# Kernel optimization log

Measured on AMD Instinct MI355X. Metric: run time of the kernel, lower is better.

The kernel has to match this reference:

```python
import jax, jax.numpy as jnp
import numpy as np

N_NODES = 200000
N_EDGES = 640000
D_NODE = 128   # NO_NODE_FEATURES_TWO
D_EDGE = 32    # NO_EDGE_FEATURES_TWO
HIDDEN = 128   # HIDDEN_NODE_TWO


def setup_inputs() -> dict:
    key = jax.random.key(0)
    ks = jax.random.split(key, 8)
    x = jax.random.normal(ks[0], (N_NODES, D_NODE), dtype=jnp.float32)
    edge_index = jax.random.randint(ks[1], (2, N_EDGES), 0, N_NODES, dtype=jnp.int64)
    edge_attr = jax.random.normal(ks[2], (N_EDGES, D_EDGE), dtype=jnp.float32)
    u = jax.random.normal(ks[3], (64, D_NODE), dtype=jnp.float32)
    batch = jax.random.randint(ks[4], (N_NODES,), 0, 64, dtype=jnp.int64)
    # Xavier-uniform linear weights (stored as [in, out]); bias filled with 0.01 as in init_weights
    def xavier(k, fan_in, fan_out):
        limit = float(np.sqrt(6.0 / (fan_in + fan_out)))
        return jax.random.uniform(k, (fan_in, fan_out), jnp.float32, -limit, limit)
    W1 = xavier(ks[5], D_EDGE + D_NODE, HIDDEN)          # [160, 128]
    b1 = jnp.full((HIDDEN,), 0.01, dtype=jnp.float32)
    W2 = xavier(ks[6], HIDDEN + D_NODE, D_NODE)          # [256, 128]
    b2 = jnp.full((D_NODE,), 0.01, dtype=jnp.float32)
    return {"x": x, "edge_index": edge_index, "edge_attr": edge_attr,
            "u": u, "batch": batch, "W1": W1, "b1": b1, "W2": W2, "b2": b2}


def reference(x, edge_index, edge_attr, u, batch, W1, b1, W2, b2):
    row, col = edge_index[0], edge_index[1]
    # gather source-node features, concat with edge features: [E, 160]
    msg = jnp.concatenate([x[row], edge_attr], axis=1)
    msg = msg @ W1 + b1                                   # [E, hidden]
    # scatter_add by destination node
    agg = jax.ops.segment_sum(msg, col, num_segments=x.shape[0])  # [N, hidden]
    out = jnp.concatenate([x, agg], axis=1)               # [N, 256]
    return out @ W2 + b2                                  # [N, 128]
```

## Files before the change

### kernel.cpp

```cpp
#include <hip/hip_runtime.h>
#include <hip/hip_bf16.h>

#define N_NODES 200000
#define N_EDGES 640000
#define D_NODE 128
#define D_EDGE 32
#define HIDDEN 128
#define KTOT 288

using bf16x8  = __attribute__((ext_vector_type(8))) short;
using f32x4   = __attribute__((ext_vector_type(4))) float;
using short4v = __attribute__((ext_vector_type(4))) short;

__device__ __forceinline__ short f2b(float f) {
  return __builtin_bit_cast(short, __float2bfloat16(f));
}
__device__ __forceinline__ float b2f(short s) {
  unsigned u = ((unsigned)(unsigned short)s) << 16;
  return __builtin_bit_cast(float, u);
}

#define PREP_NB 12500
#define HIST_NB 2500
#define WC_NB   145

__global__ __launch_bounds__(256) void k_prep(
    const float* __restrict__ x, short* __restrict__ AF,
    const int* __restrict__ ei, int* cnt, int* slot,
    const float* __restrict__ W1, const float* __restrict__ b1,
    const float* __restrict__ W2, short* __restrict__ WcT,
    float* __restrict__ bc)
{
  const int b = blockIdx.x;
  if (b < PREP_NB) {
    const int i = b * 256 + threadIdx.x;
    const int node = i >> 4;
    const int oct  = (i & 15) << 3;
    const float4 v0 = *(const float4*)&x[(size_t)node * D_NODE + oct];
    const float4 v1 = *(const float4*)&x[(size_t)node * D_NODE + oct + 4];
    bf16x8 o = { f2b(v0.x), f2b(v0.y), f2b(v0.z), f2b(v0.w),
                 f2b(v1.x), f2b(v1.y), f2b(v1.z), f2b(v1.w) };
    *(bf16x8*)&AF[(size_t)node * KTOT + oct] = o;
  } else if (b < PREP_NB + HIST_NB) {
    const int e = (b - PREP_NB) * 256 + threadIdx.x;
    slot[e] = atomicAdd(&cnt[ei[N_EDGES + e]], 1);
  } else {
    const int t = (b - PREP_NB - HIST_NB) * 256 + threadIdx.x;
    if (t < 288 * 128) {
      const int brow = t >> 7, c = t & 127;
      if (brow < 128) {
        WcT[c * KTOT + brow] = f2b(W2[brow * 128 + c]);
      } else {
        const int i = brow - 128;
        float acc = 0.f;
        #pragma unroll 8
        for (int q = 0; q < 128; ++q)
          acc += W1[i * 128 + q] * W2[(128 + q) * 128 + c];
        WcT[c * KTOT + brow] = f2b(acc);
      }
    } else if (t < 288 * 128 + 128) {
      const int c = t - 288 * 128;
      float acc = 0.f;
      #pragma unroll 8
      for (int q = 0; q < 128; ++q)
        acc += b1[q] * W2[(128 + q) * 128 + c];
      bc[c] = acc;
    }
  }
}

#define SCAN_NB 196

__global__ __launch_bounds__(256) void k_scan_a(const int* __restrict__ cnt,
                                                int* bsum) {
  __shared__ int sh[256];
  const int b = blockIdx.x, t = threadIdx.x;
  const int base = b * 1024 + t * 4;
  int s = 0;
  #pragma unroll
  for (int k = 0; k < 4; ++k) {
    const int idx = base + k;
    s += (idx < N_NODES) ? cnt[idx] : 0;
  }
  sh[t] = s; __syncthreads();
  for (int o = 128; o > 0; o >>= 1) {
    if (t < o) sh[t] += sh[t + o];
    __syncthreads();
  }
  if (t == 0) bsum[b] = sh[0];
}

__global__ __launch_bounds__(256) void k_scan_c2(const int* __restrict__ cnt,
                                                 const int* __restrict__ bsum,
                                                 int* offv) {
  __shared__ int sh[256];
  __shared__ int base_sh;
  const int b = blockIdx.x, t = threadIdx.x;

  sh[t] = (t < SCAN_NB && t < b) ? bsum[t] : 0;
  __syncthreads();
  for (int o = 128; o > 0; o >>= 1) {
    if (t < o) sh[t] += sh[t + o];
    __syncthreads();
  }
  if (t == 0) base_sh = sh[0];
  __syncthreads();

  const int base = b * 1024 + t * 4;
  int v[4], p[4], s = 0;
  #pragma unroll
  for (int k = 0; k < 4; ++k) {
    const int idx = base + k;
    v[k] = (idx < N_NODES) ? cnt[idx] : 0;
    p[k] = s; s += v[k];
  }
  sh[t] = s; __syncthreads();
  const int tot = s;
  for (int o = 1; o < 256; o <<= 1) {
    const int tv = (t >= o) ? sh[t - o] : 0;
    __syncthreads();
    sh[t] += tv;
    __syncthreads();
  }
  const int gb = base_sh + (sh[t] - tot);
  #pragma unroll
  for (int k = 0; k < 4; ++k) {
    const int idx = base + k;
    if (idx < N_NODES) offv[idx] = gb + p[k];
  }
}

__global__ __launch_bounds__(256) void k_place3(const int* __restrict__ ei,
                                                const int* __restrict__ offv,
                                                const int* __restrict__ slot,
                                                int2* __restrict__ pr) {
  const int e = blockIdx.x * 256 + threadIdx.x;
  if (e < N_EDGES) {
    const int j = offv[ei[N_EDGES + e]] + slot[e];
    int2 v; v.x = ei[e]; v.y = e;
    pr[j] = v;
  }
}

__global__ __launch_bounds__(256) void k_sagg(
    const float* __restrict__ ea, const int* __restrict__ offv,
    const int* __restrict__ cnt, const int2* __restrict__ pr,
    short* __restrict__ AF)
{
  const int gtid = blockIdx.x * 256 + threadIdx.x;
  if (gtid < N_NODES * 16) {
    const int node = gtid >> 4;
    const int oct  = (gtid & 15) << 3;
    const int s0 = offv[node];
    const int s1 = s0 + cnt[node];
    float a[8] = {};
    int j = s0;
    for (; j + 1 < s1; j += 2) {
      const int r0 = pr[j].x;
      const int r1 = pr[j + 1].x;
      const bf16x8 v0 = *(const bf16x8*)&AF[(size_t)r0 * KTOT + oct];
      const bf16x8 v1 = *(const bf16x8*)&AF[(size_t)r1 * KTOT + oct];
      #pragma unroll
      for (int k = 0; k < 8; ++k) a[k] += b2f(v0[k]) + b2f(v1[k]);
    }
    if (j < s1) {
      const bf16x8 v = *(const bf16x8*)&AF[(size_t)pr[j].x * KTOT + oct];
      #pragma unroll
      for (int k = 0; k < 8; ++k) a[k] += b2f(v[k]);
    }
    bf16x8 o;
    #pragma unroll
    for (int k = 0; k < 8; ++k) o[k] = f2b(a[k]);
    *(bf16x8*)&AF[(size_t)node * KTOT + 128 + oct] = o;
  } else {
    const int t2 = gtid - N_NODES * 16;
    const int node = t2 >> 3;
    const int q    = (t2 & 7) << 2;
    if (node >= N_NODES) return;
    const int s0 = offv[node];
    const int s1 = s0 + cnt[node];
    float a0 = 0.f, a1 = 0.f, a2 = 0.f, a3 = 0.f;
    for (int j = s0; j < s1; ++j) {
      const float4 v = *(const float4*)&ea[(size_t)pr[j].y * D_EDGE + q];
      a0 += v.x; a1 += v.y; a2 += v.z; a3 += v.w;
    }
    short4v o = { f2b(a0), f2b(a1), f2b(a2), f2b(a3) };
    *(short4v*)&AF[(size_t)node * KTOT + 256 + q] = o;
  }
}

#define LDP 104

__global__ __launch_bounds__(256, 4) void k_out2(
    const short* __restrict__ AF, const short* __restrict__ WcT,
    const float* __restrict__ bc, const float* __restrict__ b2,
    const int* __restrict__ cnt, float* __restrict__ out)
{
  __shared__ short smem[64 * LDP + 128 * LDP];
  short* lA = smem;
  short* lB = smem + 64 * LDP;
  const int tid = threadIdx.x;
  const int n0  = blockIdx.x * 64;

  const int lane = tid & 63;
  const int wid  = tid >> 6;
  const int wm = wid >> 1, wn = wid & 1;
  const int lrow = lane & 15;
  const int lk   = (lane >> 4) << 3;

  f32x4 acc[2][4] = {};

  #pragma unroll
  for (int p = 0; p < 3; ++p) {
    for (int i = tid; i < 1536; i += 256) {
      const int n = i / 12, ck = (i % 12) << 3;
      *(bf16x8*)&lB[n * LDP + ck] = *(const bf16x8*)&WcT[n * KTOT + p * 96 + ck];
    }
    for (int i = tid; i < 768; i += 256) {
      const int m = i / 12, ck = (i % 12) << 3;
      *(bf16x8*)&lA[m * LDP + ck] = *(const bf16x8*)&AF[(size_t)(n0 + m) * KTOT + p * 96 + ck];
    }
    __syncthreads();
    #pragma unroll
    for (int kt = 0; kt < 3; ++kt) {
      const int ks = kt * 32 + lk;
      bf16x8 af[2], bfr[4];
      #pragma unroll
      for (int i = 0; i < 2; ++i)
        af[i]  = *(const bf16x8*)&lA[(wm * 32 + i * 16 + lrow) * LDP + ks];
      #pragma unroll
      for (int j = 0; j < 4; ++j)
        bfr[j] = *(const bf16x8*)&lB[(wn * 64 + j * 16 + lrow) * LDP + ks];
      #pragma unroll
      for (int i = 0; i < 2; ++i)
        #pragma unroll
        for (int j = 0; j < 4; ++j)
          acc[i][j] = __builtin_amdgcn_mfma_f32_16x16x32_bf16(af[i], bfr[j], acc[i][j], 0, 0, 0);
    }
    __syncthreads();
  }

  float* lf = (float*)smem;
  const int rb = wm * 32 + ((lane >> 4) << 2);
  const int cb = wn * 64 + lrow;
  float bcv[4], b2v[4];
  #pragma unroll
  for (int j = 0; j < 4; ++j) {
    bcv[j] = bc[cb + j * 16];
    b2v[j] = b2[cb + j * 16];
  }
  #pragma unroll
  for (int i = 0; i < 2; ++i) {
    #pragma unroll
    for (int r = 0; r < 4; ++r) {
      const int row = rb + i * 16 + r;
      const float cf = (float)cnt[n0 + row];
      #pragma unroll
      for (int j = 0; j < 4; ++j)
        lf[row * 128 + cb + j * 16] = acc[i][j][r] + cf * bcv[j] + b2v[j];
    }
  }
  __syncthreads();
  #pragma unroll
  for (int u = 0; u < 8; ++u) {
    const int idx = tid + u * 256;
    const int row = idx >> 5, f4 = (idx & 31) << 2;
    *(float4*)&out[(size_t)(n0 + row) * HIDDEN + f4] = *(const float4*)&lf[row * 128 + f4];
  }
}

extern "C" void kernel_launch(void* const* d_in, const int* in_sizes, int n_in,
                              void* d_out, int out_size, void* d_ws, size_t ws_size,
                              hipStream_t stream) {
  const float* x  = (const float*)d_in[0];
  const int*   ei = (const int*)d_in[1];
  const float* ea = (const float*)d_in[2];
  const float* W1 = (const float*)d_in[5];
  const float* b1 = (const float*)d_in[6];
  const float* W2 = (const float*)d_in[7];
  const float* b2 = (const float*)d_in[8];
  float* out = (float*)d_out;

  const size_t AF_B   = (size_t)N_NODES * KTOT * 2;
  const size_t WCT_B  = 128 * KTOT * 2;
  const size_t BC_B   = 512;
  const size_t CNT_B  = (size_t)N_NODES * 4;
  const size_t SLOT_B = (size_t)N_EDGES * 4;
  const size_t PR_B   = (size_t)N_EDGES * 8;

  const size_t o_AF   = 0;
  const size_t o_wct  = o_AF + AF_B;
  const size_t o_bc   = o_wct + WCT_B;
  const size_t o_cnt  = o_bc + BC_B;
  const size_t o_off  = o_cnt + CNT_B;
  const size_t o_slot = o_off + CNT_B;
  const size_t o_pr   = o_slot + SLOT_B;
  const size_t o_bsum = o_pr + PR_B;

  short* AF   = (short*)((char*)d_ws + o_AF);
  short* WcT  = (short*)((char*)d_ws + o_wct);
  float* bc   = (float*)((char*)d_ws + o_bc);
  int*   cnt  = (int*)((char*)d_ws + o_cnt);
  int*   offv = (int*)((char*)d_ws + o_off);
  int*   slot = (int*)((char*)d_ws + o_slot);
  int2*  pr   = (int2*)((char*)d_ws + o_pr);
  int*   bsum = (int*)((char*)d_ws + o_bsum);

  hipMemsetAsync(cnt, 0, CNT_B, stream);
  k_prep<<<PREP_NB + HIST_NB + WC_NB, 256, 0, stream>>>(
      x, AF, ei, cnt, slot, W1, b1, W2, WcT, bc);

  k_scan_a <<<SCAN_NB, 256, 0, stream>>>(cnt, bsum);
  k_scan_c2<<<SCAN_NB, 256, 0, stream>>>(cnt, bsum, offv);
  k_place3 <<<(N_EDGES + 255) / 256, 256, 0, stream>>>(ei, offv, slot, pr);

  k_sagg<<<(N_NODES * 24 + 255) / 256, 256, 0, stream>>>(ea, offv, cnt, pr, AF);
  k_out2<<<N_NODES / 64, 256, 0, stream>>>(AF, WcT, bc, b2, cnt, out);
}
```

Measured before the change: 214.3 us.

## Aggregate edges per 32-node block with shared-memory atomics instead of per-node threads

```diff
diff --git a/kernel.cpp b/kernel.cpp
--- a/kernel.cpp
+++ b/kernel.cpp
@@ -130,62 +130,70 @@
   }
 }
 
-__global__ __launch_bounds__(256) void k_place3(const int* __restrict__ ei,
+__global__ __launch_bounds__(256) void k_place4(const int* __restrict__ ei,
                                                 const int* __restrict__ offv,
                                                 const int* __restrict__ slot,
                                                 int2* __restrict__ pr) {
   const int e = blockIdx.x * 256 + threadIdx.x;
   if (e < N_EDGES) {
-    const int j = offv[ei[N_EDGES + e]] + slot[e];
-    int2 v; v.x = ei[e]; v.y = e;
+    const int dst = ei[N_EDGES + e];
+    const int j = offv[dst] + slot[e];
+    int2 v;
+    v.x = ei[e] | ((dst & 31) << 18);
+    v.y = e;
     pr[j] = v;
   }
 }
 
-__global__ __launch_bounds__(256) void k_sagg(
+#define SG_NB 32
+#define SG_LD 168
+
+__global__ __launch_bounds__(256) void k_sagg2(
     const float* __restrict__ ea, const int* __restrict__ offv,
-    const int* __restrict__ cnt, const int2* __restrict__ pr,
-    short* __restrict__ AF)
+    const int2* __restrict__ pr, short* __restrict__ AF)
 {
-  const int gtid = blockIdx.x * 256 + threadIdx.x;
-  if (gtid < N_NODES * 16) {
-    const int node = gtid >> 4;
-    const int oct  = (gtid & 15) << 3;
-    const int s0 = offv[node];
-    const int s1 = s0 + cnt[node];
-    float a[8] = {};
-    int j = s0;
-    for (; j + 1 < s1; j += 2) {
-      const int r0 = pr[j].x;
-      const int r1 = pr[j + 1].x;
-      const bf16x8 v0 = *(const bf16x8*)&AF[(size_t)r0 * KTOT + oct];
-      const bf16x8 v1 = *(const bf16x8*)&AF[(size_t)r1 * KTOT + oct];
-      #pragma unroll
-      for (int k = 0; k < 8; ++k) a[k] += b2f(v0[k]) + b2f(v1[k]);
-    }
-    if (j < s1) {
-      const bf16x8 v = *(const bf16x8*)&AF[(size_t)pr[j].x * KTOT + oct];
-      #pragma unroll
-      for (int k = 0; k < 8; ++k) a[k] += b2f(v[k]);
-    }
-    bf16x8 o;
+  __shared__ float acc[SG_NB][SG_LD];
+  const int tid = threadIdx.x;
+  const int b   = blockIdx.x;
+  const int n0  = b * SG_NB;
+  const int jlo = offv[n0];
+  const int jhi = (b == (N_NODES / SG_NB) - 1) ? N_EDGES : offv[n0 + SG_NB];
+  const int count = jhi - jlo;
+
+  for (int i = tid; i < SG_NB * SG_LD; i += 256) ((float*)acc)[i] = 0.f;
+  __syncthreads();
+
+  for (int idx = tid; idx < count * 16; idx += 256) {
+    const int j   = jlo + (idx >> 4);
+    const int oct = (idx & 15) << 3;
+    const int2 w  = pr[j];
+    const int src = w.x & 0x3FFFF;
+    const int dl  = (w.x >> 18) & 31;
+    const bf16x8 v = *(const bf16x8*)&AF[(size_t)src * KTOT + oct];
     #pragma unroll
-    for (int k = 0; k < 8; ++k) o[k] = f2b(a[k]);
-    *(bf16x8*)&AF[(size_t)node * KTOT + 128 + oct] = o;
-  } else {
-    const int t2 = gtid - N_NODES * 16;
-    const int node = t2 >> 3;
-    const int q    = (t2 & 7) << 2;
-    if (node >= N_NODES) return;
-    const int s0 = offv[node];
-    const int s1 = s0 + cnt[node];
-    float a0 = 0.f, a1 = 0.f, a2 = 0.f, a3 = 0.f;
-    for (int j = s0; j < s1; ++j) {
-      const float4 v = *(const float4*)&ea[(size_t)pr[j].y * D_EDGE + q];
-      a0 += v.x; a1 += v.y; a2 += v.z; a3 += v.w;
-    }
-    short4v o = { f2b(a0), f2b(a1), f2b(a2), f2b(a3) };
-    *(short4v*)&AF[(size_t)node * KTOT + 256 + q] = o;
+    for (int k = 0; k < 8; ++k)
+      atomicAdd(&acc[dl][oct + k], b2f(v[k]));
+  }
+  for (int idx = tid; idx < count * 8; idx += 256) {
+    const int j  = jlo + (idx >> 3);
+    const int q  = (idx & 7) << 2;
+    const int2 w = pr[j];
+    const int dl = (w.x >> 18) & 31;
+    const float4 v = *(const float4*)&ea[(size_t)w.y * D_EDGE + q];
+    atomicAdd(&acc[dl][128 + q + 0], v.x);
+    atomicAdd(&acc[dl][128 + q + 1], v.y);
+    atomicAdd(&acc[dl][128 + q + 2], v.z);
+    atomicAdd(&acc[dl][128 + q + 3], v.w);
+  }
+  __syncthreads();
+
+  for (int i = tid; i < SG_NB * 20; i += 256) {
+    const int m  = i / 20;
+    const int c8 = (i % 20) << 3;
+    bf16x8 v;
+    #pragma unroll
+    for (int k = 0; k < 8; ++k) v[k] = f2b(acc[m][c8 + k]);
+    *(bf16x8*)&AF[(size_t)(n0 + m) * KTOT + 128 + c8] = v;
   }
 }
 
@@ -312,8 +320,8 @@
 
   k_scan_a <<<SCAN_NB, 256, 0, stream>>>(cnt, bsum);
   k_scan_c2<<<SCAN_NB, 256, 0, stream>>>(cnt, bsum, offv);
-  k_place3 <<<(N_EDGES + 255) / 256, 256, 0, stream>>>(ei, offv, slot, pr);
-
-  k_sagg<<<(N_NODES * 24 + 255) / 256, 256, 0, stream>>>(ea, offv, cnt, pr, AF);
-  k_out2<<<N_NODES / 64, 256, 0, stream>>>(AF, WcT, bc, b2, cnt, out);
-}
+  k_place4 <<<(N_EDGES + 255) / 256, 256, 0, stream>>>(ei, offv, slot, pr);
+
+  k_sagg2<<<N_NODES / SG_NB, 256, 0, stream>>>(ea, offv, pr, AF);
+  k_out2 <<<N_NODES / 64, 256, 0, stream>>>(AF, WcT, bc, b2, cnt, out);
+}
```

After: 681.7 us. 218% more time.

## Pre-permute edge features to bf16 in CSR order and unroll gather by four

Applied to the files above, without the earlier changes.

```diff
diff --git a/kernel.cpp b/kernel.cpp
--- a/kernel.cpp
+++ b/kernel.cpp
@@ -130,62 +130,82 @@
   }
 }
 
-__global__ __launch_bounds__(256) void k_place3(const int* __restrict__ ei,
-                                                const int* __restrict__ offv,
-                                                const int* __restrict__ slot,
-                                                int2* __restrict__ pr) {
+__global__ __launch_bounds__(256) void k_place5(
+    const int* __restrict__ ei, const int* __restrict__ offv,
+    const int* __restrict__ slot, const float* __restrict__ ea,
+    int* __restrict__ psrc, short* __restrict__ ea_s)
+{
   const int e = blockIdx.x * 256 + threadIdx.x;
   if (e < N_EDGES) {
     const int j = offv[ei[N_EDGES + e]] + slot[e];
-    int2 v; v.x = ei[e]; v.y = e;
-    pr[j] = v;
-  }
-}
-
-__global__ __launch_bounds__(256) void k_sagg(
-    const float* __restrict__ ea, const int* __restrict__ offv,
-    const int* __restrict__ cnt, const int2* __restrict__ pr,
+    psrc[j] = ei[e];
+    #pragma unroll
+    for (int h = 0; h < 4; ++h) {
+      const float4 w0 = *(const float4*)&ea[(size_t)e * D_EDGE + h * 8];
+      const float4 w1 = *(const float4*)&ea[(size_t)e * D_EDGE + h * 8 + 4];
+      bf16x8 o = { f2b(w0.x), f2b(w0.y), f2b(w0.z), f2b(w0.w),
+                   f2b(w1.x), f2b(w1.y), f2b(w1.z), f2b(w1.w) };
+      *(bf16x8*)&ea_s[(size_t)j * D_EDGE + h * 8] = o;
+    }
+  }
+}
+
+__global__ __launch_bounds__(256) void k_sagg4(
+    const int* __restrict__ offv, const int* __restrict__ cnt,
+    const int* __restrict__ psrc, const short* __restrict__ ea_s,
     short* __restrict__ AF)
 {
   const int gtid = blockIdx.x * 256 + threadIdx.x;
   if (gtid < N_NODES * 16) {
     const int node = gtid >> 4;
-    const int oct  = (gtid & 15) << 3;
+    const int oct8 = (gtid & 15) << 3;
     const int s0 = offv[node];
     const int s1 = s0 + cnt[node];
     float a[8] = {};
     int j = s0;
-    for (; j + 1 < s1; j += 2) {
-      const int r0 = pr[j].x;
-      const int r1 = pr[j + 1].x;
-      const bf16x8 v0 = *(const bf16x8*)&AF[(size_t)r0 * KTOT + oct];
-      const bf16x8 v1 = *(const bf16x8*)&AF[(size_t)r1 * KTOT + oct];
-      #pragma unroll
-      for (int k = 0; k < 8; ++k) a[k] += b2f(v0[k]) + b2f(v1[k]);
-    }
-    if (j < s1) {
-      const bf16x8 v = *(const bf16x8*)&AF[(size_t)pr[j].x * KTOT + oct];
-      #pragma unroll
-      for (int k = 0; k < 8; ++k) a[k] += b2f(v[k]);
+    while (j < s1) {
+      const int rem = s1 - j;
+      bf16x8 v0, v1, v2, v3;
+      v0 = *(const bf16x8*)&AF[(size_t)psrc[j] * KTOT + oct8];
+      if (rem > 1) v1 = *(const bf16x8*)&AF[(size_t)psrc[j + 1] * KTOT + oct8];
+      if (rem > 2) v2 = *(const bf16x8*)&AF[(size_t)psrc[j + 2] * KTOT + oct8];
+      if (rem > 3) v3 = *(const bf16x8*)&AF[(size_t)psrc[j + 3] * KTOT + oct8];
+      #pragma unroll
+      for (int k = 0; k < 8; ++k) a[k] += b2f(v0[k]);
+      if (rem > 1) {
+        #pragma unroll
+        for (int k = 0; k < 8; ++k) a[k] += b2f(v1[k]);
+      }
+      if (rem > 2) {
+        #pragma unroll
+        for (int k = 0; k < 8; ++k) a[k] += b2f(v2[k]);
+      }
+      if (rem > 3) {
+        #pragma unroll
+        for (int k = 0; k < 8; ++k) a[k] += b2f(v3[k]);
+      }
+      j += 4;
     }
     bf16x8 o;
     #pragma unroll
     for (int k = 0; k < 8; ++k) o[k] = f2b(a[k]);
-    *(bf16x8*)&AF[(size_t)node * KTOT + 128 + oct] = o;
+    *(bf16x8*)&AF[(size_t)node * KTOT + 128 + oct8] = o;
   } else {
     const int t2 = gtid - N_NODES * 16;
-    const int node = t2 >> 3;
-    const int q    = (t2 & 7) << 2;
-    if (node >= N_NODES) return;
+    const int node = t2 >> 2;
+    const int q8   = (t2 & 3) << 3;
     const int s0 = offv[node];
     const int s1 = s0 + cnt[node];
-    float a0 = 0.f, a1 = 0.f, a2 = 0.f, a3 = 0.f;
+    float a[8] = {};
     for (int j = s0; j < s1; ++j) {
-      const float4 v = *(const float4*)&ea[(size_t)pr[j].y * D_EDGE + q];
-      a0 += v.x; a1 += v.y; a2 += v.z; a3 += v.w;
-    }
-    short4v o = { f2b(a0), f2b(a1), f2b(a2), f2b(a3) };
-    *(short4v*)&AF[(size_t)node * KTOT + 256 + q] = o;
+      const bf16x8 v = *(const bf16x8*)&ea_s[(size_t)j * D_EDGE + q8];
+      #pragma unroll
+      for (int k = 0; k < 8; ++k) a[k] += b2f(v[k]);
+    }
+    bf16x8 o;
+    #pragma unroll
+    for (int k = 0; k < 8; ++k) o[k] = f2b(a[k]);
+    *(bf16x8*)&AF[(size_t)node * KTOT + 256 + q8] = o;
   }
 }
 
@@ -286,7 +306,8 @@
   const size_t BC_B   = 512;
   const size_t CNT_B  = (size_t)N_NODES * 4;
   const size_t SLOT_B = (size_t)N_EDGES * 4;
-  const size_t PR_B   = (size_t)N_EDGES * 8;
+  const size_t PSRC_B = (size_t)N_EDGES * 4;
+  const size_t EAS_B  = (size_t)N_EDGES * D_EDGE * 2;
 
   const size_t o_AF   = 0;
   const size_t o_wct  = o_AF + AF_B;
@@ -294,8 +315,9 @@
   const size_t o_cnt  = o_bc + BC_B;
   const size_t o_off  = o_cnt + CNT_B;
   const size_t o_slot = o_off + CNT_B;
-  const size_t o_pr   = o_slot + SLOT_B;
-  const size_t o_bsum = o_pr + PR_B;
+  const size_t o_psrc = o_slot + SLOT_B;
+  const size_t o_eas  = o_psrc + PSRC_B;
+  const size_t o_bsum = o_eas + EAS_B;
 
   short* AF   = (short*)((char*)d_ws + o_AF);
   short* WcT  = (short*)((char*)d_ws + o_wct);
@@ -303,7 +325,8 @@
   int*   cnt  = (int*)((char*)d_ws + o_cnt);
   int*   offv = (int*)((char*)d_ws + o_off);
   int*   slot = (int*)((char*)d_ws + o_slot);
-  int2*  pr   = (int2*)((char*)d_ws + o_pr);
+  int*   psrc = (int*)((char*)d_ws + o_psrc);
+  short* ea_s = (short*)((char*)d_ws + o_eas);
   int*   bsum = (int*)((char*)d_ws + o_bsum);
 
   hipMemsetAsync(cnt, 0, CNT_B, stream);
@@ -312,8 +335,8 @@
 
   k_scan_a <<<SCAN_NB, 256, 0, stream>>>(cnt, bsum);
   k_scan_c2<<<SCAN_NB, 256, 0, stream>>>(cnt, bsum, offv);
-  k_place3 <<<(N_EDGES + 255) / 256, 256, 0, stream>>>(ei, offv, slot, pr);
-
-  k_sagg<<<(N_NODES * 24 + 255) / 256, 256, 0, stream>>>(ea, offv, cnt, pr, AF);
-  k_out2<<<N_NODES / 64, 256, 0, stream>>>(AF, WcT, bc, b2, cnt, out);
-}
+  k_place5 <<<(N_EDGES + 255) / 256, 256, 0, stream>>>(ei, offv, slot, ea, psrc, ea_s);
+
+  k_sagg4<<<(N_NODES * 20) / 256, 256, 0, stream>>>(offv, cnt, psrc, ea_s, AF);
+  k_out2 <<<N_NODES / 64, 256, 0, stream>>>(AF, WcT, bc, b2, cnt, out);
+}
```

Result: slower. 224.6 us (+4.8%).
